# Kernel optimization log

Hardware: AMD Instinct MI355X
Metric: run time of the kernel (lower is better)

## Reference

```python
import jax, jax.numpy as jnp
import numpy as np

B, T, C, H = 2, 2048, 1024, 16
HD = C // H  # head dim = 64


def setup_inputs() -> dict:
    key = jax.random.key(0)
    ks = jax.random.split(key, 5)
    scale = 0.02
    return {
        "x": jax.random.normal(ks[0], (B, T, C), dtype=jnp.float32),
        "W_attn": jax.random.normal(ks[1], (C, 3 * C), dtype=jnp.float32) * scale,
        "b_attn": jax.random.normal(ks[2], (3 * C,), dtype=jnp.float32) * scale,
        "W_proj": jax.random.normal(ks[3], (C, C), dtype=jnp.float32) * scale,
        "b_proj": jax.random.normal(ks[4], (C,), dtype=jnp.float32) * scale,
    }


def reference(x, W_attn, b_attn, W_proj, b_proj):
    Bd, Td, Cd = x.shape
    qkv = x @ W_attn + b_attn                      # [B,T,3C]
    q, k, v = jnp.split(qkv, 3, axis=-1)           # each [B,T,C]
    # [B,T,C] -> [B,H,T,HD]
    def heads(t):
        return t.reshape(Bd, Td, H, HD).transpose(0, 2, 1, 3)
    q, k, v = heads(q), heads(k), heads(v)
    att = jnp.einsum('bhqd,bhkd->bhqk', q, k) * (1.0 / np.sqrt(HD))
    causal = jnp.tril(jnp.ones((Td, Td), dtype=bool))
    att = jnp.where(causal[None, None, :, :], att, -jnp.inf)
    att = jax.nn.softmax(att, axis=-1)
    y = jnp.einsum('bhqk,bhkd->bhqd', att, v)      # [B,H,T,HD]
    y = y.transpose(0, 2, 1, 3).reshape(Bd, Td, Cd)
    return y @ W_proj + b_proj
```

## Files before the change

kernel.cpp:

```cpp
#include <hip/hip_runtime.h>
#include <hip/hip_bf16.h>


typedef __attribute__((ext_vector_type(8))) __bf16 bf16x8;
typedef __attribute__((ext_vector_type(8))) short short8;
typedef __attribute__((ext_vector_type(4))) short short4v;
typedef __attribute__((ext_vector_type(4))) float floatx4;
typedef __attribute__((ext_vector_type(2))) __fp16 fp16x2;
typedef __attribute__((ext_vector_type(4))) _Float16 half4v;

__device__ __forceinline__ unsigned short f2b(float f) {
    unsigned int x = __float_as_uint(f);
    x += 0x7fffu + ((x >> 16) & 1u);
    return (unsigned short)(x >> 16);
}
__device__ __forceinline__ half4v pack4h(float a, float b, float c, float d) {
    union { fp16x2 c2[2]; half4v h4; } u;
    u.c2[0] = __builtin_amdgcn_cvt_pkrtz(a, b);
    u.c2[1] = __builtin_amdgcn_cvt_pkrtz(c, d);
    return u.h4;
}
__device__ __forceinline__ void gld16(const void* g, void* l) {
    __builtin_amdgcn_global_load_lds((const __attribute__((address_space(1))) void*)g,
                                     (__attribute__((address_space(3))) void*)l, 16, 0, 0);
}

__global__ __launch_bounds__(256) void prep_k(
    const float* __restrict__ x,  unsigned short* __restrict__ xb,
    const float* __restrict__ Wa, unsigned short* __restrict__ WTa,
    const float* __restrict__ Wp, unsigned short* __restrict__ WTp)
{
    __shared__ unsigned short tl[64][72];
    const int id = blockIdx.x, t = threadIdx.x;

    if (id < 2048) {
        int i = (id * 256 + t) << 3;
        const float4 a = *(const float4*)(x + i);
        const float4 b = *(const float4*)(x + i + 4);
        short8 v;
        v[0] = (short)f2b(a.x); v[1] = (short)f2b(a.y);
        v[2] = (short)f2b(a.z); v[3] = (short)f2b(a.w);
        v[4] = (short)f2b(b.x); v[5] = (short)f2b(b.y);
        v[6] = (short)f2b(b.z); v[7] = (short)f2b(b.w);
        *(short8*)(xb + i) = v;
        return;
    }

    const float* in;
    unsigned short* out;
    int R, Cc, bx, by;
    if (id < 2816) {
        in = Wa; out = WTa; R = 1024; Cc = 3072;
        bx = (id - 2048) % 48; by = (id - 2048) / 48;
    } else {
        in = Wp; out = WTp; R = 1024; Cc = 1024;
        bx = (id - 2816) % 16; by = (id - 2816) / 16;
    }
    const int r0 = by * 64, c0 = bx * 64;
#pragma unroll
    for (int it = 0; it < 2; ++it) {
        int idx = it * 256 + t, r = idx >> 3, c8 = (idx & 7) << 3;
        const float* p = in + (size_t)(r0 + r) * Cc + c0 + c8;
        const float4 a = *(const float4*)p;
        const float4 b = *(const float4*)(p + 4);
        tl[r][c8 + 0] = f2b(a.x); tl[r][c8 + 1] = f2b(a.y);
        tl[r][c8 + 2] = f2b(a.z); tl[r][c8 + 3] = f2b(a.w);
        tl[r][c8 + 4] = f2b(b.x); tl[r][c8 + 5] = f2b(b.y);
        tl[r][c8 + 6] = f2b(b.z); tl[r][c8 + 7] = f2b(b.w);
    }
    __syncthreads();
#pragma unroll
    for (int it = 0; it < 2; ++it) {
        int idx = it * 256 + t, rr = idx >> 3, c8 = (idx & 7) << 3;
        short8 v;
#pragma unroll
        for (int i = 0; i < 8; ++i) v[i] = (short)tl[c8 + i][rr];
        *(short8*)(out + (size_t)(c0 + rr) * R + r0 + c8) = v;
    }
}

__global__ __launch_bounds__(256) void gemm_qkv(
    const unsigned short* __restrict__ A,
    const unsigned short* __restrict__ BT,
    const float* __restrict__ bias,
    unsigned short* __restrict__ outqk,
    unsigned short* __restrict__ outvt)
{
    __shared__ __align__(16) unsigned short SM[2][2][128][32];
    unsigned short* Esc = &SM[0][0][0][0];

    const int t = threadIdx.x;
    const int w = t >> 6, lane = t & 63, l15 = lane & 15, quad = lane >> 4;
    const int wr = w >> 1, wc = w & 1;
    const int m0 = blockIdx.y * 128, n0 = blockIdx.x * 128;
    const int K = 1024;

    float bia[4];
#pragma unroll
    for (int j = 0; j < 4; ++j) bia[j] = bias[n0 + wc * 64 + j * 16 + l15];

    floatx4 acc[4][4];
#pragma unroll
    for (int i = 0; i < 4; ++i)
#pragma unroll
        for (int j = 0; j < 4; ++j) acc[i][j] = (floatx4)0.f;

    const int row_s = t >> 2, kg_s = (t & 3) << 3;
    const unsigned short* gA = A  + (size_t)(m0 + row_s) * K + kg_s;
    const unsigned short* gB = BT + (size_t)(n0 + row_s) * K + kg_s;
    const int ldst = (w * 64) * 8;

#pragma unroll
    for (int c = 0; c < 2; ++c) {
        gld16(gA + (size_t)c * 64 * K, &SM[0][0][0][0] + c * 2048 + ldst);
        gld16(gB + (size_t)c * 64 * K, &SM[0][1][0][0] + c * 2048 + ldst);
    }

    for (int it = 0; it < 32; ++it) {
        __syncthreads();
        const int cur = it & 1;
        if (it < 31) {
            const int k0 = (it + 1) * 32;
#pragma unroll
            for (int c = 0; c < 2; ++c) {
                gld16(gA + (size_t)c * 64 * K + k0, &SM[cur ^ 1][0][0][0] + c * 2048 + ldst);
                gld16(gB + (size_t)c * 64 * K + k0, &SM[cur ^ 1][1][0][0] + c * 2048 + ldst);
            }
        }
        bf16x8 af[4], bfr[4];
#pragma unroll
        for (int i = 0; i < 4; ++i) af[i] = *(const bf16x8*)&SM[cur][0][wr * 64 + i * 16 + l15][quad * 8];
#pragma unroll
        for (int j = 0; j < 4; ++j) bfr[j] = *(const bf16x8*)&SM[cur][1][wc * 64 + j * 16 + l15][quad * 8];
#pragma unroll
        for (int i = 0; i < 4; ++i)
#pragma unroll
            for (int j = 0; j < 4; ++j)
                acc[i][j] = __builtin_amdgcn_mfma_f32_16x16x32_bf16(af[i], bfr[j], acc[i][j], 0, 0, 0);
    }

    const int bb = m0 >> 11, tbase = m0 & 2047;
    if (n0 < 2048) {
        for (int cf = 0; cf < 2; ++cf) {
            const int fb = n0 + cf * 64;
            const int which = fb >> 10, h = (fb & 1023) >> 6;
            const float scl = (which == 0) ? 0.18033688011112042f : 1.0f;
            __syncthreads();
            if (wc == cf) {
#pragma unroll
                for (int i = 0; i < 4; ++i)
#pragma unroll
                    for (int j = 0; j < 4; ++j)
#pragma unroll
                        for (int r = 0; r < 4; ++r)
                            Esc[(wr * 64 + i * 16 + quad * 4 + r) * 72 + j * 16 + l15] =
                                f2b((acc[i][j][r] + bia[j]) * scl);
            }
            __syncthreads();
            const int row = t >> 1, co = (t & 1) << 5;
            const unsigned short* src = Esc + row * 72 + co;
            unsigned short* dst = outqk + (size_t)which * 4194304
                + (((size_t)(bb * 16 + h) * 2048 + tbase + row) * 64 + co);
#pragma unroll
            for (int u = 0; u < 4; ++u)
                *(short8*)(dst + u * 8) = *(const short8*)(src + u * 8);
        }
    } else {
        const int hb = (n0 & 1023) >> 6;
        for (int hf = 0; hf < 2; ++hf) {
            __syncthreads();
            if (wr == hf) {
#pragma unroll
                for (int i = 0; i < 4; ++i)
#pragma unroll
                    for (int j = 0; j < 4; ++j) {
                        half4v hp = pack4h(acc[i][j][0] + bia[j], acc[i][j][1] + bia[j],
                                           acc[i][j][2] + bia[j], acc[i][j][3] + bia[j]);
                        *(half4v*)&Esc[(wc * 64 + j * 16 + l15) * 72 + i * 16 + quad * 4] = hp;
                    }
            }
            __syncthreads();
            const int dl = t >> 1, co = (t & 1) << 5;
            const int h = hb + (dl >> 6), d = dl & 63;
            const unsigned short* src = Esc + dl * 72 + co;
            unsigned short* dst = outvt
                + (((size_t)(bb * 16 + h) * 64 + d) * 2048 + tbase + hf * 64 + co);
#pragma unroll
            for (int u = 0; u < 4; ++u)
                *(short8*)(dst + u * 8) = *(const short8*)(src + u * 8);
        }
    }
}

__global__ __launch_bounds__(256) void gemm_proj(
    const unsigned short* __restrict__ A,
    const unsigned short* __restrict__ BT,
    const float* __restrict__ bias,
    float* __restrict__ outf)
{
    __shared__ __align__(16) unsigned short SM[2][2][128][32];
    float* Ef = (float*)&SM[0][0][0][0];

    const int t = threadIdx.x;
    const int w = t >> 6, lane = t & 63, l15 = lane & 15, quad = lane >> 4;
    const int wr = w >> 1, wc = w & 1;
    const int m0 = blockIdx.y * 128, n0 = blockIdx.x * 128;
    const int K = 1024, N = 1024;

    float bia[4];
#pragma unroll
    for (int j = 0; j < 4; ++j) bia[j] = bias[n0 + wc * 64 + j * 16 + l15];

    floatx4 acc[4][4];
#pragma unroll
    for (int i = 0; i < 4; ++i)
#pragma unroll
        for (int j = 0; j < 4; ++j) acc[i][j] = (floatx4)0.f;

    const int row_s = t >> 2, kg_s = (t & 3) << 3;
    const unsigned short* gA = A  + (size_t)(m0 + row_s) * K + kg_s;
    const unsigned short* gB = BT + (size_t)(n0 + row_s) * K + kg_s;
    const int ldst = (w * 64) * 8;

#pragma unroll
    for (int c = 0; c < 2; ++c) {
        gld16(gA + (size_t)c * 64 * K, &SM[0][0][0][0] + c * 2048 + ldst);
        gld16(gB + (size_t)c * 64 * K, &SM[0][1][0][0] + c * 2048 + ldst);
    }

    for (int it = 0; it < 32; ++it) {
        __syncthreads();
        const int cur = it & 1;
        if (it < 31) {
            const int k0 = (it + 1) * 32;
#pragma unroll
            for (int c = 0; c < 2; ++c) {
                gld16(gA + (size_t)c * 64 * K + k0, &SM[cur ^ 1][0][0][0] + c * 2048 + ldst);
                gld16(gB + (size_t)c * 64 * K + k0, &SM[cur ^ 1][1][0][0] + c * 2048 + ldst);
            }
        }
        bf16x8 af[4], bfr[4];
#pragma unroll
        for (int i = 0; i < 4; ++i) af[i] = *(const bf16x8*)&SM[cur][0][wr * 64 + i * 16 + l15][quad * 8];
#pragma unroll
        for (int j = 0; j < 4; ++j) bfr[j] = *(const bf16x8*)&SM[cur][1][wc * 64 + j * 16 + l15][quad * 8];
#pragma unroll
        for (int i = 0; i < 4; ++i)
#pragma unroll
            for (int j = 0; j < 4; ++j)
                acc[i][j] = __builtin_amdgcn_mfma_f32_16x16x32_bf16(af[i], bfr[j], acc[i][j], 0, 0, 0);
    }

    for (int qf = 0; qf < 4; ++qf) {
        __syncthreads();
        if (wr == (qf >> 1)) {
            const int ib = (qf & 1) * 2;
#pragma unroll
            for (int ii = 0; ii < 2; ++ii)
#pragma unroll
                for (int j = 0; j < 4; ++j)
#pragma unroll
                    for (int r = 0; r < 4; ++r)
                        Ef[(ii * 16 + quad * 4 + r) * 132 + wc * 64 + j * 16 + l15] =
                            acc[ib + ii][j][r] + bia[j];
        }
        __syncthreads();
        const int row = t >> 3, co = (t & 7) << 4;
        const float* src = Ef + row * 132 + co;
        float* dst = outf + (size_t)(m0 + qf * 32 + row) * N + n0 + co;
#pragma unroll
        for (int u = 0; u < 4; ++u)
            *(float4*)(dst + u * 4) = *(const float4*)(src + u * 4);
    }
}

__global__ __launch_bounds__(256) void attn_k(
    const unsigned short* __restrict__ qg,
    const unsigned short* __restrict__ kg,
    const unsigned short* __restrict__ vt,
    unsigned short* __restrict__ y)
{
    __shared__ unsigned short Kb[2][64][64];
    __shared__ unsigned short Vb[2][64][64];

    const int t = threadIdx.x, w = t >> 6, lane = t & 63;
    const int l15 = lane & 15, quad = lane >> 4;
    const int id = blockIdx.x;
    const int s = id >> 3;
    const int bh = (id & 7) * 4 + (s & 3);
    const int p = 15 - (s >> 2);
    const int b = bh >> 4, h = bh & 15;
    const int q0 = p * 128 + w * 32;
    const int ktend = 2 * p + 2;

    const half4v onesh = {(_Float16)1.f, (_Float16)1.f, (_Float16)1.f, (_Float16)1.f};

    bf16x8 Qf[2][2];
#pragma unroll
    for (int qb = 0; qb < 2; ++qb) {
        const unsigned short* qrow = qg + ((size_t)bh * 2048 + q0 + qb * 16 + l15) * 64 + quad * 8;
        Qf[qb][0] = *(const bf16x8*)(qrow);
        Qf[qb][1] = *(const bf16x8*)(qrow + 32);
    }

    floatx4 OT[2][4];
#pragma unroll
    for (int qb = 0; qb < 2; ++qb)
#pragma unroll
        for (int jd = 0; jd < 4; ++jd) OT[qb][jd] = (floatx4)0.f;
    floatx4 lacc[2];
    lacc[0] = (floatx4)0.f; lacc[1] = (floatx4)0.f;

    const int r_s = t >> 3, g_s = t & 7;

#pragma unroll
    for (int c = 0; c < 2; ++c) {
        int r = c * 32 + r_s;
        int cg = (g_s ^ (r & 7)) << 3;
        gld16(kg + ((size_t)bh * 2048 + r) * 64 + cg, &Kb[0][0][0] + (size_t)(c * 256 + w * 64) * 8);
        gld16(vt + ((size_t)bh * 64 + r) * 2048 + cg, &Vb[0][0][0] + (size_t)(c * 256 + w * 64) * 8);
    }

#pragma unroll 1
    for (int kt = 0; kt < ktend; ++kt) {
        __syncthreads();
        const int cur = kt & 1;
        if (kt + 1 < ktend) {
            const int kbase = (kt + 1) * 64, nxt = cur ^ 1;
#pragma unroll
            for (int c = 0; c < 2; ++c) {
                int r = c * 32 + r_s;
                int cg = (g_s ^ (r & 7)) << 3;
                gld16(kg + ((size_t)bh * 2048 + kbase + r) * 64 + cg,
                      &Kb[nxt][0][0] + (size_t)(c * 256 + w * 64) * 8);
                gld16(vt + ((size_t)bh * 64 + r) * 2048 + kbase + cg,
                      &Vb[nxt][0][0] + (size_t)(c * 256 + w * 64) * 8);
            }
        }

#pragma unroll
        for (int jk = 0; jk < 4; ++jk) {
            bf16x8 Kf0 = *(const bf16x8*)&Kb[cur][jk * 16 + l15][((0 * 4 + quad) ^ (l15 & 7)) << 3];
            bf16x8 Kf1 = *(const bf16x8*)&Kb[cur][jk * 16 + l15][((1 * 4 + quad) ^ (l15 & 7)) << 3];
            half4v Vf[4];
#pragma unroll
            for (int jd = 0; jd < 4; ++jd) {
                const int pc = ((((2 * jk) + (quad >> 1)) ^ (l15 & 7)) << 3) + (quad & 1) * 4;
                Vf[jd] = *(const half4v*)&Vb[cur][jd * 16 + l15][pc];
            }

#pragma unroll
            for (int qb = 0; qb < 2; ++qb) {
                const int qlo = q0 + qb * 16;
                if (kt * 64 > qlo + 15) continue;

                floatx4 st = (floatx4)0.f;
                st = __builtin_amdgcn_mfma_f32_16x16x32_bf16(Kf0, Qf[qb][0], st, 0, 0, 0);
                st = __builtin_amdgcn_mfma_f32_16x16x32_bf16(Kf1, Qf[qb][1], st, 0, 0, 0);

                float e[4];
                const int kb_ = kt * 64 + jk * 16 + quad * 4;
                const int qg_ = qlo + l15;
                if (kt * 64 + 63 > qlo) {
#pragma unroll
                    for (int r = 0; r < 4; ++r)
                        e[r] = (kb_ + r > qg_) ? 0.f : exp2f(st[r]);
                } else {
#pragma unroll
                    for (int r = 0; r < 4; ++r) e[r] = exp2f(st[r]);
                }
                half4v Pf = pack4h(e[0], e[1], e[2], e[3]);

                lacc[qb] = __builtin_amdgcn_mfma_f32_16x16x16f16(onesh, Pf, lacc[qb], 0, 0, 0);
#pragma unroll
                for (int jd = 0; jd < 4; ++jd)
                    OT[qb][jd] = __builtin_amdgcn_mfma_f32_16x16x16f16(Vf[jd], Pf, OT[qb][jd], 0, 0, 0);
            }
        }
    }

#pragma unroll
    for (int qb = 0; qb < 2; ++qb) {
        const float inv = 1.f / lacc[qb][0];
        const int q = q0 + qb * 16 + l15;
#pragma unroll
        for (int jd = 0; jd < 4; ++jd) {
            short4v o;
#pragma unroll
            for (int r = 0; r < 4; ++r) o[r] = (short)f2b(OT[qb][jd][r] * inv);
            *(short4v*)(y + ((size_t)b * 2048 + q) * 1024 + h * 64 + jd * 16 + quad * 4) = o;
        }
    }
}

extern "C" void kernel_launch(void* const* d_in, const int* in_sizes, int n_in,
                              void* d_out, int out_size, void* d_ws, size_t ws_size,
                              hipStream_t stream) {
    const float* x      = (const float*)d_in[0];
    const float* W_attn = (const float*)d_in[1];
    const float* b_attn = (const float*)d_in[2];
    const float* W_proj = (const float*)d_in[3];
    const float* b_proj = (const float*)d_in[4];
    float* out = (float*)d_out;

    char* ws = (char*)d_ws;
    unsigned short* qk  = (unsigned short*)(ws);
    unsigned short* vtb = (unsigned short*)(ws + 16777216);
    unsigned short* y   = (unsigned short*)(ws + 25165824);
    unsigned short* xb  = (unsigned short*)(ws + 33554432);
    unsigned short* WTa = (unsigned short*)(ws + 41943040);
    unsigned short* WTp = (unsigned short*)(ws + 48234496);

    prep_k<<<3072, 256, 0, stream>>>(x, xb, W_attn, WTa, W_proj, WTp);
    gemm_qkv<<<dim3(24, 32), 256, 0, stream>>>(xb, WTa, b_attn, qk, vtb);
    attn_k<<<512, 256, 0, stream>>>(qk, qk + 4194304, vtb, y);
    gemm_proj<<<dim3(8, 32), 256, 0, stream>>>(y, WTp, b_proj, out);
}
```

Measured before the change: 221.2 us.

## Split attention keys across waves with LDS reduction and paired causal tiles

The attention kernel is restructured. Each block now handles a 64-query tile and its mirror tile (p and 31-p) to balance causal work. The four waves split each 64-key chunk, 16 keys apiece, and load K/V straight from global memory into registers with a one-chunk prefetch. The old LDS double buffering and per-iteration barriers are gone, replaced by a final cross-wave reduction of partial O and row sums through shared memory. This cuts block-wide syncs and evens out per-block load, at the cost of more register pressure (16 accumulators), uncoalesced direct global loads, and extra reduction traffic.

```diff
diff --git a/kernel.cpp b/kernel.cpp
--- a/kernel.cpp
+++ b/kernel.cpp
@@ -280,91 +280,83 @@
     const unsigned short* __restrict__ vt,
     unsigned short* __restrict__ y)
 {
-    __shared__ unsigned short Kb[2][64][64];
-    __shared__ unsigned short Vb[2][64][64];
+    __shared__ float Ored[2 * 5120];
 
     const int t = threadIdx.x, w = t >> 6, lane = t & 63;
     const int l15 = lane & 15, quad = lane >> 4;
     const int id = blockIdx.x;
-    const int s = id >> 3;
-    const int bh = (id & 7) * 4 + (s & 3);
-    const int p = 15 - (s >> 2);
+    const int bh = (id & 7) * 4 + ((id >> 3) & 3);
+    const int p = id >> 5;
     const int b = bh >> 4, h = bh & 15;
-    const int q0 = p * 128 + w * 32;
-    const int ktend = 2 * p + 2;
 
     const half4v onesh = {(_Float16)1.f, (_Float16)1.f, (_Float16)1.f, (_Float16)1.f};
-
-    bf16x8 Qf[2][2];
-#pragma unroll
-    for (int qb = 0; qb < 2; ++qb) {
-        const unsigned short* qrow = qg + ((size_t)bh * 2048 + q0 + qb * 16 + l15) * 64 + quad * 8;
-        Qf[qb][0] = *(const bf16x8*)(qrow);
-        Qf[qb][1] = *(const bf16x8*)(qrow + 32);
-    }
-
-    floatx4 OT[2][4];
-#pragma unroll
-    for (int qb = 0; qb < 2; ++qb)
-#pragma unroll
-        for (int jd = 0; jd < 4; ++jd) OT[qb][jd] = (floatx4)0.f;
-    floatx4 lacc[2];
-    lacc[0] = (floatx4)0.f; lacc[1] = (floatx4)0.f;
-
-    const int r_s = t >> 3, g_s = t & 7;
-
-#pragma unroll
-    for (int c = 0; c < 2; ++c) {
-        int r = c * 32 + r_s;
-        int cg = (g_s ^ (r & 7)) << 3;
-        gld16(kg + ((size_t)bh * 2048 + r) * 64 + cg, &Kb[0][0][0] + (size_t)(c * 256 + w * 64) * 8);
-        gld16(vt + ((size_t)bh * 64 + r) * 2048 + cg, &Vb[0][0][0] + (size_t)(c * 256 + w * 64) * 8);
-    }
+    const unsigned short* kwave = kg + (size_t)bh * 2048 * 64 + (w * 16 + l15) * 64;
 
 #pragma unroll 1
-    for (int kt = 0; kt < ktend; ++kt) {
-        __syncthreads();
-        const int cur = kt & 1;
-        if (kt + 1 < ktend) {
-            const int kbase = (kt + 1) * 64, nxt = cur ^ 1;
-#pragma unroll
-            for (int c = 0; c < 2; ++c) {
-                int r = c * 32 + r_s;
-                int cg = (g_s ^ (r & 7)) << 3;
-                gld16(kg + ((size_t)bh * 2048 + kbase + r) * 64 + cg,
-                      &Kb[nxt][0][0] + (size_t)(c * 256 + w * 64) * 8);
-                gld16(vt + ((size_t)bh * 64 + r) * 2048 + kbase + cg,
-                      &Vb[nxt][0][0] + (size_t)(c * 256 + w * 64) * 8);
-            }
-        }
-
-#pragma unroll
-        for (int jk = 0; jk < 4; ++jk) {
-            bf16x8 Kf0 = *(const bf16x8*)&Kb[cur][jk * 16 + l15][((0 * 4 + quad) ^ (l15 & 7)) << 3];
-            bf16x8 Kf1 = *(const bf16x8*)&Kb[cur][jk * 16 + l15][((1 * 4 + quad) ^ (l15 & 7)) << 3];
-            half4v Vf[4];
-#pragma unroll
-            for (int jd = 0; jd < 4; ++jd) {
-                const int pc = ((((2 * jk) + (quad >> 1)) ^ (l15 & 7)) << 3) + (quad & 1) * 4;
-                Vf[jd] = *(const half4v*)&Vb[cur][jd * 16 + l15][pc];
-            }
-
-#pragma unroll
-            for (int qb = 0; qb < 2; ++qb) {
-                const int qlo = q0 + qb * 16;
-                if (kt * 64 > qlo + 15) continue;
+    for (int hv = 0; hv < 2; ++hv) {
+        const int qt = hv ? (31 - p) : p;
+        const int qbase = qt * 64;
+
+        bf16x8 Qf[4][2];
+#pragma unroll
+        for (int qb = 0; qb < 4; ++qb) {
+            const unsigned short* qrow =
+                qg + ((size_t)bh * 2048 + qbase + qb * 16 + l15) * 64 + quad * 8;
+            Qf[qb][0] = *(const bf16x8*)(qrow);
+            Qf[qb][1] = *(const bf16x8*)(qrow + 32);
+        }
+
+        floatx4 OT[4][4];
+        floatx4 lacc[4];
+#pragma unroll
+        for (int qb = 0; qb < 4; ++qb) {
+            lacc[qb] = (floatx4)0.f;
+#pragma unroll
+            for (int jd = 0; jd < 4; ++jd) OT[qb][jd] = (floatx4)0.f;
+        }
+
+        bf16x8 Kc[2];
+        half4v Vc[4];
+        {
+            const unsigned short* kp = kwave;
+            Kc[0] = *(const bf16x8*)(kp + quad * 8);
+            Kc[1] = *(const bf16x8*)(kp + 32 + quad * 8);
+#pragma unroll
+            for (int jd = 0; jd < 4; ++jd)
+                Vc[jd] = *(const half4v*)(vt + ((size_t)bh * 64 + jd * 16 + l15) * 2048
+                                          + w * 16 + quad * 4);
+        }
+
+#pragma unroll 1
+        for (int kt = 0; kt <= qt; ++kt) {
+            const int knb = (kt < qt ? kt + 1 : qt) * 64;
+            bf16x8 Kn[2];
+            half4v Vn[4];
+            {
+                const unsigned short* kp = kwave + (size_t)knb * 64;
+                Kn[0] = *(const bf16x8*)(kp + quad * 8);
+                Kn[1] = *(const bf16x8*)(kp + 32 + quad * 8);
+#pragma unroll
+                for (int jd = 0; jd < 4; ++jd)
+                    Vn[jd] = *(const half4v*)(vt + ((size_t)bh * 64 + jd * 16 + l15) * 2048
+                                              + knb + w * 16 + quad * 4);
+            }
+
+            const bool diag = (kt == qt);
+#pragma unroll
+            for (int qb = 0; qb < 4; ++qb) {
+                if (diag && qb < w) continue;
 
                 floatx4 st = (floatx4)0.f;
-                st = __builtin_amdgcn_mfma_f32_16x16x32_bf16(Kf0, Qf[qb][0], st, 0, 0, 0);
-                st = __builtin_amdgcn_mfma_f32_16x16x32_bf16(Kf1, Qf[qb][1], st, 0, 0, 0);
+                st = __builtin_amdgcn_mfma_f32_16x16x32_bf16(Kc[0], Qf[qb][0], st, 0, 0, 0);
+                st = __builtin_amdgcn_mfma_f32_16x16x32_bf16(Kc[1], Qf[qb][1], st, 0, 0, 0);
 
                 float e[4];
-                const int kb_ = kt * 64 + jk * 16 + quad * 4;
-                const int qg_ = qlo + l15;
-                if (kt * 64 + 63 > qlo) {
+                if (diag && qb == w) {
+                    const int kl = quad * 4, ql = l15;
 #pragma unroll
                     for (int r = 0; r < 4; ++r)
-                        e[r] = (kb_ + r > qg_) ? 0.f : exp2f(st[r]);
+                        e[r] = (kl + r > ql) ? 0.f : exp2f(st[r]);
                 } else {
 #pragma unroll
                     for (int r = 0; r < 4; ++r) e[r] = exp2f(st[r]);
@@ -374,21 +366,68 @@
                 lacc[qb] = __builtin_amdgcn_mfma_f32_16x16x16f16(onesh, Pf, lacc[qb], 0, 0, 0);
 #pragma unroll
                 for (int jd = 0; jd < 4; ++jd)
-                    OT[qb][jd] = __builtin_amdgcn_mfma_f32_16x16x16f16(Vf[jd], Pf, OT[qb][jd], 0, 0, 0);
-            }
-        }
-    }
-
-#pragma unroll
-    for (int qb = 0; qb < 2; ++qb) {
-        const float inv = 1.f / lacc[qb][0];
-        const int q = q0 + qb * 16 + l15;
-#pragma unroll
-        for (int jd = 0; jd < 4; ++jd) {
-            short4v o;
-#pragma unroll
-            for (int r = 0; r < 4; ++r) o[r] = (short)f2b(OT[qb][jd][r] * inv);
-            *(short4v*)(y + ((size_t)b * 2048 + q) * 1024 + h * 64 + jd * 16 + quad * 4) = o;
+                    OT[qb][jd] = __builtin_amdgcn_mfma_f32_16x16x16f16(Vc[jd], Pf, OT[qb][jd], 0, 0, 0);
+            }
+
+#pragma unroll
+            for (int kk = 0; kk < 2; ++kk) Kc[kk] = Kn[kk];
+#pragma unroll
+            for (int jd = 0; jd < 4; ++jd) Vc[jd] = Vn[jd];
+        }
+
+        __syncthreads();
+        if (w >= 2) {
+            float* s = Ored + (w - 2) * 5120;
+#pragma unroll
+            for (int qb = 0; qb < 4; ++qb) {
+#pragma unroll
+                for (int jd = 0; jd < 4; ++jd)
+                    *(floatx4*)(s + ((qb * 5 + jd) * 64 + lane) * 4) = OT[qb][jd];
+                *(floatx4*)(s + ((qb * 5 + 4) * 64 + lane) * 4) = lacc[qb];
+            }
+        }
+        __syncthreads();
+        if (w < 2) {
+            const float* s = Ored + w * 5120;
+#pragma unroll
+            for (int qb = 0; qb < 4; ++qb) {
+#pragma unroll
+                for (int jd = 0; jd < 4; ++jd)
+                    OT[qb][jd] += *(const floatx4*)(s + ((qb * 5 + jd) * 64 + lane) * 4);
+                lacc[qb] += *(const floatx4*)(s + ((qb * 5 + 4) * 64 + lane) * 4);
+            }
+            float* d = Ored + w * 5120;
+            const int qlo = (w == 0) ? 2 : 0;
+#pragma unroll
+            for (int q2 = 0; q2 < 2; ++q2) {
+                const int qb = qlo + q2;
+#pragma unroll
+                for (int jd = 0; jd < 4; ++jd)
+                    *(floatx4*)(d + ((qb * 5 + jd) * 64 + lane) * 4) = OT[qb][jd];
+                *(floatx4*)(d + ((qb * 5 + 4) * 64 + lane) * 4) = lacc[qb];
+            }
+        }
+        __syncthreads();
+        if (w < 2) {
+            const float* s = Ored + (1 - w) * 5120;
+            const int qlo = (w == 0) ? 0 : 2;
+#pragma unroll
+            for (int q2 = 0; q2 < 2; ++q2) {
+                const int qb = qlo + q2;
+#pragma unroll
+                for (int jd = 0; jd < 4; ++jd)
+                    OT[qb][jd] += *(const floatx4*)(s + ((qb * 5 + jd) * 64 + lane) * 4);
+                lacc[qb] += *(const floatx4*)(s + ((qb * 5 + 4) * 64 + lane) * 4);
+                const float inv = 1.f / lacc[qb][0];
+                const int q = qbase + qb * 16 + l15;
+#pragma unroll
+                for (int jd = 0; jd < 4; ++jd) {
+                    short4v o;
+#pragma unroll
+                    for (int r = 0; r < 4; ++r) o[r] = (short)f2b(OT[qb][jd][r] * inv);
+                    *(short4v*)(y + ((size_t)b * 2048 + q) * 1024 + h * 64 + jd * 16 + quad * 4) = o;
+                }
+            }
         }
     }
 }
```

Measured after the change: 325.0 us. 1.47x slower.

## Pair light and heavy 64-row query tiles per block for causal load balance

Applied to the files above, without the earlier changes.

Each attention block now handles two 64-row query tiles, p and 31-p, one after the other, so every block does about the same amount of causal work. This replaces the previous 128-row tiles ordered heaviest first. Each wave now owns 16 query rows instead of 32, and fully masked 16-key sub-tiles on the diagonal are skipped per wave. K/V tiles are reloaded for each half and each wave keeps half as many accumulators, which lowers register pressure but also reduces K/V reuse from shared memory.

```diff
diff --git a/kernel.cpp b/kernel.cpp
--- a/kernel.cpp
+++ b/kernel.cpp
@@ -286,108 +286,100 @@
     const int t = threadIdx.x, w = t >> 6, lane = t & 63;
     const int l15 = lane & 15, quad = lane >> 4;
     const int id = blockIdx.x;
-    const int s = id >> 3;
-    const int bh = (id & 7) * 4 + (s & 3);
-    const int p = 15 - (s >> 2);
+    const int bh = (id & 7) * 4 + ((id >> 3) & 3);
+    const int p = id >> 5;
     const int b = bh >> 4, h = bh & 15;
-    const int q0 = p * 128 + w * 32;
-    const int ktend = 2 * p + 2;
 
     const half4v onesh = {(_Float16)1.f, (_Float16)1.f, (_Float16)1.f, (_Float16)1.f};
-
-    bf16x8 Qf[2][2];
-#pragma unroll
-    for (int qb = 0; qb < 2; ++qb) {
-        const unsigned short* qrow = qg + ((size_t)bh * 2048 + q0 + qb * 16 + l15) * 64 + quad * 8;
-        Qf[qb][0] = *(const bf16x8*)(qrow);
-        Qf[qb][1] = *(const bf16x8*)(qrow + 32);
-    }
-
-    floatx4 OT[2][4];
-#pragma unroll
-    for (int qb = 0; qb < 2; ++qb)
-#pragma unroll
-        for (int jd = 0; jd < 4; ++jd) OT[qb][jd] = (floatx4)0.f;
-    floatx4 lacc[2];
-    lacc[0] = (floatx4)0.f; lacc[1] = (floatx4)0.f;
-
     const int r_s = t >> 3, g_s = t & 7;
 
-#pragma unroll
-    for (int c = 0; c < 2; ++c) {
-        int r = c * 32 + r_s;
-        int cg = (g_s ^ (r & 7)) << 3;
-        gld16(kg + ((size_t)bh * 2048 + r) * 64 + cg, &Kb[0][0][0] + (size_t)(c * 256 + w * 64) * 8);
-        gld16(vt + ((size_t)bh * 64 + r) * 2048 + cg, &Vb[0][0][0] + (size_t)(c * 256 + w * 64) * 8);
-    }
-
 #pragma unroll 1
-    for (int kt = 0; kt < ktend; ++kt) {
+    for (int hv = 0; hv < 2; ++hv) {
+        const int qt = hv ? (31 - p) : p;
+        const int qbase = qt * 64;
+
+        bf16x8 Qf[2];
+        {
+            const unsigned short* qrow =
+                qg + ((size_t)bh * 2048 + qbase + w * 16 + l15) * 64 + quad * 8;
+            Qf[0] = *(const bf16x8*)(qrow);
+            Qf[1] = *(const bf16x8*)(qrow + 32);
+        }
+
+        floatx4 OT[4];
+        floatx4 lacc = (floatx4)0.f;
+#pragma unroll
+        for (int jd = 0; jd < 4; ++jd) OT[jd] = (floatx4)0.f;
+
         __syncthreads();
-        const int cur = kt & 1;
-        if (kt + 1 < ktend) {
-            const int kbase = (kt + 1) * 64, nxt = cur ^ 1;
-#pragma unroll
-            for (int c = 0; c < 2; ++c) {
-                int r = c * 32 + r_s;
-                int cg = (g_s ^ (r & 7)) << 3;
-                gld16(kg + ((size_t)bh * 2048 + kbase + r) * 64 + cg,
-                      &Kb[nxt][0][0] + (size_t)(c * 256 + w * 64) * 8);
-                gld16(vt + ((size_t)bh * 64 + r) * 2048 + kbase + cg,
-                      &Vb[nxt][0][0] + (size_t)(c * 256 + w * 64) * 8);
-            }
-        }
-
-#pragma unroll
-        for (int jk = 0; jk < 4; ++jk) {
-            bf16x8 Kf0 = *(const bf16x8*)&Kb[cur][jk * 16 + l15][((0 * 4 + quad) ^ (l15 & 7)) << 3];
-            bf16x8 Kf1 = *(const bf16x8*)&Kb[cur][jk * 16 + l15][((1 * 4 + quad) ^ (l15 & 7)) << 3];
-            half4v Vf[4];
-#pragma unroll
-            for (int jd = 0; jd < 4; ++jd) {
-                const int pc = ((((2 * jk) + (quad >> 1)) ^ (l15 & 7)) << 3) + (quad & 1) * 4;
-                Vf[jd] = *(const half4v*)&Vb[cur][jd * 16 + l15][pc];
-            }
-
-#pragma unroll
-            for (int qb = 0; qb < 2; ++qb) {
-                const int qlo = q0 + qb * 16;
-                if (kt * 64 > qlo + 15) continue;
+#pragma unroll
+        for (int c = 0; c < 2; ++c) {
+            int r = c * 32 + r_s;
+            int cg = (g_s ^ (r & 7)) << 3;
+            gld16(kg + ((size_t)bh * 2048 + r) * 64 + cg,
+                  &Kb[0][0][0] + (size_t)(c * 256 + w * 64) * 8);
+            gld16(vt + ((size_t)bh * 64 + r) * 2048 + cg,
+                  &Vb[0][0][0] + (size_t)(c * 256 + w * 64) * 8);
+        }
+
+#pragma unroll 1
+        for (int kt = 0; kt <= qt; ++kt) {
+            __syncthreads();
+            const int cur = kt & 1;
+            if (kt < qt) {
+                const int kbase = (kt + 1) * 64, nxt = cur ^ 1;
+#pragma unroll
+                for (int c = 0; c < 2; ++c) {
+                    int r = c * 32 + r_s;
+                    int cg = (g_s ^ (r & 7)) << 3;
+                    gld16(kg + ((size_t)bh * 2048 + kbase + r) * 64 + cg,
+                          &Kb[nxt][0][0] + (size_t)(c * 256 + w * 64) * 8);
+                    gld16(vt + ((size_t)bh * 64 + r) * 2048 + kbase + cg,
+                          &Vb[nxt][0][0] + (size_t)(c * 256 + w * 64) * 8);
+                }
+            }
+
+            const bool diag = (kt == qt);
+#pragma unroll
+            for (int jk = 0; jk < 4; ++jk) {
+                if (diag && jk > w) continue;
+
+                bf16x8 Kf0 = *(const bf16x8*)&Kb[cur][jk * 16 + l15][((quad) ^ (l15 & 7)) << 3];
+                bf16x8 Kf1 = *(const bf16x8*)&Kb[cur][jk * 16 + l15][((4 + quad) ^ (l15 & 7)) << 3];
 
                 floatx4 st = (floatx4)0.f;
-                st = __builtin_amdgcn_mfma_f32_16x16x32_bf16(Kf0, Qf[qb][0], st, 0, 0, 0);
-                st = __builtin_amdgcn_mfma_f32_16x16x32_bf16(Kf1, Qf[qb][1], st, 0, 0, 0);
+                st = __builtin_amdgcn_mfma_f32_16x16x32_bf16(Kf0, Qf[0], st, 0, 0, 0);
+                st = __builtin_amdgcn_mfma_f32_16x16x32_bf16(Kf1, Qf[1], st, 0, 0, 0);
 
                 float e[4];
-                const int kb_ = kt * 64 + jk * 16 + quad * 4;
-                const int qg_ = qlo + l15;
-                if (kt * 64 + 63 > qlo) {
+                if (diag && jk == w) {
+                    const int kl = jk * 16 + quad * 4, ql = w * 16 + l15;
 #pragma unroll
                     for (int r = 0; r < 4; ++r)
-                        e[r] = (kb_ + r > qg_) ? 0.f : exp2f(st[r]);
+                        e[r] = (kl + r > ql) ? 0.f : exp2f(st[r]);
                 } else {
 #pragma unroll
                     for (int r = 0; r < 4; ++r) e[r] = exp2f(st[r]);
                 }
                 half4v Pf = pack4h(e[0], e[1], e[2], e[3]);
 
-                lacc[qb] = __builtin_amdgcn_mfma_f32_16x16x16f16(onesh, Pf, lacc[qb], 0, 0, 0);
-#pragma unroll
-                for (int jd = 0; jd < 4; ++jd)
-                    OT[qb][jd] = __builtin_amdgcn_mfma_f32_16x16x16f16(Vf[jd], Pf, OT[qb][jd], 0, 0, 0);
-            }
-        }
-    }
-
-#pragma unroll
-    for (int qb = 0; qb < 2; ++qb) {
-        const float inv = 1.f / lacc[qb][0];
-        const int q = q0 + qb * 16 + l15;
+                lacc = __builtin_amdgcn_mfma_f32_16x16x16f16(onesh, Pf, lacc, 0, 0, 0);
+#pragma unroll
+                for (int jd = 0; jd < 4; ++jd) {
+                    const int pc = (((2 * jk + (quad >> 1)) ^ (l15 & 7)) << 3) + (quad & 1) * 4;
+                    half4v Vf = *(const half4v*)&Vb[cur][jd * 16 + l15][pc];
+                    OT[jd] = __builtin_amdgcn_mfma_f32_16x16x16f16(Vf, Pf, OT[jd], 0, 0, 0);
+                }
+            }
+        }
+
+        const float inv = 1.f / lacc[0];
+        const int q = qbase + w * 16 + l15;
 #pragma unroll
         for (int jd = 0; jd < 4; ++jd) {
             short4v o;
 #pragma unroll
-            for (int r = 0; r < 4; ++r) o[r] = (short)f2b(OT[qb][jd][r] * inv);
+            for (int r = 0; r < 4; ++r) o[r] = (short)f2b(OT[jd][r] * inv);
             *(short4v*)(y + ((size_t)b * 2048 + q) * 1024 + h * 64 + jd * 16 + quad * 4) = o;
         }
     }
```

After: 203.6 us. 1.09x faster.
